# Kernel optimization log

Hardware: AMD Instinct MI355X
Metric: run time of the kernel (lower is better)

The kernel has to match this reference:

```python
import jax, jax.numpy as jnp
import numpy as np

B, L, DIM, H = 2, 2048, 2048, 16
DH = DIM // H  # 128, size_per_head


def setup_inputs() -> dict:
    key = jax.random.key(0)
    k1, k2, k3, k4, k5, k6 = jax.random.split(key, 6)
    s = 0.02
    return {
        "query_tensor": jax.random.normal(k1, (B, L, DIM), jnp.float32),
        "value_tensor": jax.random.normal(k2, (B, L, DIM), jnp.float32),
        "attention_mask": jax.random.randint(k3, (B, L), 0, 2).astype(jnp.float32),
        "Wq": jax.random.normal(k4, (DIM, DIM), jnp.float32) * s,
        "Wk": jax.random.normal(k5, (DIM, DIM), jnp.float32) * s,
        "Wv": jax.random.normal(k6, (DIM, DIM), jnp.float32) * s,
    }


def reference(query_tensor, value_tensor, attention_mask, Wq, Wk, Wv):
    b, lq, dim = query_tensor.shape
    lv = value_tensor.shape[1]
    # torch Linear: x @ W.T (no bias)
    q = query_tensor @ Wq.T   # [B, Lq, DIM]
    k = value_tensor @ Wk.T   # [B, Lv, DIM]
    v = value_tensor @ Wv.T   # [B, Lv, DIM]
    # split heads -> [B, H, L, DH]
    q = q.reshape(b, lq, H, DH).transpose(0, 2, 1, 3)
    k = k.reshape(b, lv, H, DH).transpose(0, 2, 1, 3)
    v = v.reshape(b, lv, H, DH).transpose(0, 2, 1, 3)
    scores = jnp.einsum('bhqd,bhkd->bhqk', q, k) / jnp.sqrt(jnp.float32(DH))
    # multiplicative per-query mask, broadcast [B,1,Lq,1] -> [B,H,Lq,Lv]
    scores = scores * attention_mask[:, None, :, None]
    probs = jax.nn.softmax(scores, axis=-1)
    attn = jnp.einsum('bhqk,bhkd->bhqd', probs, v)  # [B,H,Lq,DH]
    return attn.transpose(0, 2, 1, 3).reshape(b, lq, dim)
```

## Files before the change

### kernel.cpp

```cpp
#include <hip/hip_runtime.h>
#include <hip/hip_bf16.h>
#include <stdint.h>

#define DIM_ 2048
#define L_   2048
#define B_   2
#define H_   16
#define DH_  128
#define NT_  32

#define QSCALE_ 0.12751743f

typedef __attribute__((ext_vector_type(4))) float fp32x4;
typedef __attribute__((ext_vector_type(8))) short s16x8;

__device__ __forceinline__ unsigned short bf16_rne(float f) {
    unsigned u = __builtin_bit_cast(unsigned, f);
    u += 0x7fffu + ((u >> 16) & 1u);
    return (unsigned short)(u >> 16);
}

__device__ __forceinline__ fp32x4 MFMA(s16x8 a, s16x8 b, fp32x4 c) {
    return __builtin_amdgcn_mfma_f32_16x16x32_bf16(a, b, c, 0, 0, 0);
}

__device__ __forceinline__ void gld16(const void* g, void* l) {
    auto gp = reinterpret_cast<const uint32_t __attribute__((address_space(1)))*>(
        reinterpret_cast<uintptr_t>(g));
    auto lp = reinterpret_cast<uint32_t __attribute__((address_space(3)))*>(
        reinterpret_cast<uintptr_t>(l));
    __builtin_amdgcn_global_load_lds(gp, lp, 16, 0, 0);
}

__device__ __forceinline__ float exp2_raw(float x) {
    float r; asm("v_exp_f32 %0, %1" : "=v"(r) : "v"(x)); return r;
}

__device__ __forceinline__ unsigned cvtpk_bf16(float a, float b) {
    unsigned r; asm("v_cvt_pk_bf16_f32 %0, %1, %2" : "=v"(r) : "v"(a), "v"(b)); return r;
}

__global__ void __launch_bounds__(256)
cvt_all(const float* __restrict__ query, const float* __restrict__ value,
        const float* __restrict__ Wq, const float* __restrict__ Wk,
        const float* __restrict__ Wv,
        unsigned short* __restrict__ qb, unsigned short* __restrict__ vb,
        unsigned short* __restrict__ wqb, unsigned short* __restrict__ wkb,
        unsigned short* __restrict__ wvb)
{
    const int total4 = 7340032;
    int i = blockIdx.x * 256 + threadIdx.x;
    const int stride = gridDim.x * 256;
    for (; i < total4; i += stride) {
        const float4* s; ushort4* d; int off; float sc = 1.0f;
        if (i < 2097152)      { s = (const float4*)query; d = (ushort4*)qb;  off = i; }
        else if (i < 4194304) { s = (const float4*)value; d = (ushort4*)vb;  off = i - 2097152; }
        else if (i < 5242880) { s = (const float4*)Wq;    d = (ushort4*)wqb; off = i - 4194304; sc = QSCALE_; }
        else if (i < 6291456) { s = (const float4*)Wk;    d = (ushort4*)wkb; off = i - 5242880; }
        else                  { s = (const float4*)Wv;    d = (ushort4*)wvb; off = i - 6291456; }
        float4 v = s[off];
        ushort4 o;
        o.x = bf16_rne(v.x * sc); o.y = bf16_rne(v.y * sc);
        o.z = bf16_rne(v.z * sc); o.w = bf16_rne(v.w * sc);
        d[off] = o;
    }
}

__global__ void __launch_bounds__(512, 2)
qgemm(const unsigned short* __restrict__ qb, const unsigned short* __restrict__ wqb,
      const float* __restrict__ mask, unsigned short* __restrict__ q_ws)
{
    __shared__ __align__(16) char As_[3][32768];
    __shared__ __align__(16) char Bs_[3][16384];

    const int tid  = threadIdx.x;
    const int lane = tid & 63;
    const int wid  = tid >> 6;
    const int wm   = wid >> 1;
    const int wn   = wid & 1;
    const int lr   = lane & 15;
    const int lg   = lane >> 4;

    const int rb = (blockIdx.x & 7) * 32 + (blockIdx.x >> 3);
    const int bm = (rb >> 4) << 8;
    const int bn = (rb & 15) << 7;

    const int srow = tid >> 3;
    const int scol = ((tid & 7) ^ ((tid >> 3) & 7)) * 8;
    const unsigned short* gA = qb  + (size_t)(bm + srow) * DIM_ + scol;
    const unsigned short* gB = wqb + (size_t)(bn + srow) * DIM_ + scol;
    const int ldst = wid * 1024;

    const int r7   = (lr & 7) << 4;
    const int arow = (wm * 64 + lr) * 128;
    const int brow = (wn * 64 + lr) * 128;
    const int off0 = (lg << 4) ^ r7;
    const int off1 = (64 | (lg << 4)) ^ r7;

    fp32x4 acc[4][4] = {};

#define STG6(SA, SB, T) do {                                                      \
    gld16(gA + (size_t)(T) * 64,                 (SA) + ldst);                    \
    gld16(gA + (size_t)64  * DIM_ + (T) * 64,    (SA) + 8192  + ldst);            \
    gld16(gA + (size_t)128 * DIM_ + (T) * 64,    (SA) + 16384 + ldst);            \
    gld16(gA + (size_t)192 * DIM_ + (T) * 64,    (SA) + 24576 + ldst);            \
    gld16(gB + (size_t)(T) * 64,                 (SB) + ldst);                    \
    gld16(gB + (size_t)64  * DIM_ + (T) * 64,    (SB) + 8192  + ldst);            \
} while (0)

    STG6(&As_[0][0], &Bs_[0][0], 0);
    STG6(&As_[1][0], &Bs_[1][0], 1);
    asm volatile("s_waitcnt vmcnt(6)" ::: "memory");
    __builtin_amdgcn_s_barrier();

    for (int t = 0; t < NT_; ++t) {
        char* Ab = &As_[t % 3][0];
        char* Bb = &Bs_[t % 3][0];
        if (t < NT_ - 2) {
            STG6(&As_[(t + 2) % 3][0], &Bs_[(t + 2) % 3][0], t + 2);
        }

        s16x8 fa0[4], fa1[4], fb0[4], fb1[4];
        #pragma unroll
        for (int mi = 0; mi < 4; ++mi) {
            fa0[mi] = *reinterpret_cast<const s16x8*>(&Ab[arow + mi * 2048 + off0]);
            fa1[mi] = *reinterpret_cast<const s16x8*>(&Ab[arow + mi * 2048 + off1]);
        }
        #pragma unroll
        for (int nf = 0; nf < 4; ++nf) {
            fb0[nf] = *reinterpret_cast<const s16x8*>(&Bb[brow + nf * 2048 + off0]);
            fb1[nf] = *reinterpret_cast<const s16x8*>(&Bb[brow + nf * 2048 + off1]);
        }

        __builtin_amdgcn_s_setprio(1);
        #pragma unroll
        for (int mi = 0; mi < 4; ++mi)
            #pragma unroll
            for (int nf = 0; nf < 4; ++nf)
                acc[mi][nf] = MFMA(fa0[mi], fb0[nf], acc[mi][nf]);
        #pragma unroll
        for (int mi = 0; mi < 4; ++mi)
            #pragma unroll
            for (int nf = 0; nf < 4; ++nf)
                acc[mi][nf] = MFMA(fa1[mi], fb1[nf], acc[mi][nf]);
        __builtin_amdgcn_s_setprio(0);

        if (t < NT_ - 2) {
            asm volatile("s_waitcnt vmcnt(6)" ::: "memory");
            __builtin_amdgcn_s_barrier();
        } else if (t == NT_ - 2) {
            asm volatile("s_waitcnt vmcnt(0)" ::: "memory");
            __builtin_amdgcn_s_barrier();
        }
    }
#undef STG6

    const int bb = bm >> 11;
    const size_t bh0 = (size_t)(bb * H_) * (L_ * DH_);
    const int rbase = bm + wm * 64;
    const int cbase = bn + wn * 64;
    const float* mrow = mask + bb * L_;

    #pragma unroll
    for (int mf = 0; mf < 4; ++mf)
        #pragma unroll
        for (int rr = 0; rr < 4; ++rr) {
            int l = (rbase + mf * 16 + lg * 4 + rr) & (L_ - 1);
            float mvv = mrow[l];
            #pragma unroll
            for (int nf = 0; nf < 4; ++nf) {
                int dc = cbase + nf * 16 + lr;
                int h = dc >> 7, d = dc & 127;
                q_ws[bh0 + (size_t)h * (L_ * DH_) + (size_t)l * DH_ + d]
                    = bf16_rne(acc[mf][nf][rr] * mvv);
            }
        }
}

__global__ void __launch_bounds__(512, 2)
kvgemm(const unsigned short* __restrict__ vb, const unsigned short* __restrict__ wkb,
       const unsigned short* __restrict__ wvb,
       unsigned short* __restrict__ k_ws, unsigned short* __restrict__ v_ws)
{
    __shared__ __align__(16) char As_[2][32768];
    __shared__ __align__(16) char Bks_[2][16384];
    __shared__ __align__(16) char Bvs_[2][16384];

    const int tid  = threadIdx.x;
    const int lane = tid & 63;
    const int wid  = tid >> 6;
    const int wm   = wid >> 1;
    const int wn   = wid & 1;
    const int lr   = lane & 15;
    const int lg   = lane >> 4;

    const int rb = (blockIdx.x & 7) * 32 + (blockIdx.x >> 3);
    const int bm = (rb >> 4) << 8;
    const int bn = (rb & 15) << 7;

    const int srow = tid >> 3;
    const int scol = ((tid & 7) ^ ((tid >> 3) & 7)) * 8;
    const unsigned short* gA  = vb  + (size_t)(bm + srow) * DIM_ + scol;
    const unsigned short* gBk = wkb + (size_t)(bn + srow) * DIM_ + scol;
    const unsigned short* gBv = wvb + (size_t)(bn + srow) * DIM_ + scol;
    const int ldst = wid * 1024;

    const int r7   = (lr & 7) << 4;
    const int arow = (wm * 64 + lr) * 128;
    const int brow = (wn * 64 + lr) * 128;
    const int off0 = (lg << 4) ^ r7;
    const int off1 = (64 | (lg << 4)) ^ r7;

    fp32x4 acck[4][4] = {};
    fp32x4 accv[4][4] = {};

#define STG8(BUF, T) do {                                                         \
    gld16(gA  + (size_t)(T) * 64,               &As_[BUF][ldst]);                 \
    gld16(gA  + (size_t)64  * DIM_ + (T) * 64,  &As_[BUF][8192  + ldst]);         \
    gld16(gA  + (size_t)128 * DIM_ + (T) * 64,  &As_[BUF][16384 + ldst]);         \
    gld16(gA  + (size_t)192 * DIM_ + (T) * 64,  &As_[BUF][24576 + ldst]);         \
    gld16(gBk + (size_t)(T) * 64,               &Bks_[BUF][ldst]);                \
    gld16(gBk + (size_t)64  * DIM_ + (T) * 64,  &Bks_[BUF][8192 + ldst]);         \
    gld16(gBv + (size_t)(T) * 64,               &Bvs_[BUF][ldst]);                \
    gld16(gBv + (size_t)64  * DIM_ + (T) * 64,  &Bvs_[BUF][8192 + ldst]);         \
} while (0)

    STG8(0, 0);
    asm volatile("s_waitcnt vmcnt(0)" ::: "memory");
    __builtin_amdgcn_s_barrier();

    for (int t = 0; t < NT_; ++t) {
        const int buf = t & 1;
        if (t + 1 < NT_) STG8(buf ^ 1, t + 1);

        char* Ab  = &As_[buf][0];
        char* Bkb = &Bks_[buf][0];
        char* Bvb = &Bvs_[buf][0];

        #pragma unroll
        for (int kk = 0; kk < 2; ++kk) {
            const int o = kk ? off1 : off0;
            s16x8 fa[4], fk[4];
            #pragma unroll
            for (int mi = 0; mi < 4; ++mi)
                fa[mi] = *reinterpret_cast<const s16x8*>(&Ab[arow + mi * 2048 + o]);
            #pragma unroll
            for (int nf = 0; nf < 4; ++nf)
                fk[nf] = *reinterpret_cast<const s16x8*>(&Bkb[brow + nf * 2048 + o]);
            __builtin_amdgcn_s_setprio(1);
            #pragma unroll
            for (int mi = 0; mi < 4; ++mi)
                #pragma unroll
                for (int nf = 0; nf < 4; ++nf)
                    acck[mi][nf] = MFMA(fa[mi], fk[nf], acck[mi][nf]);
            __builtin_amdgcn_s_setprio(0);
            s16x8 fv[4];
            #pragma unroll
            for (int nf = 0; nf < 4; ++nf)
                fv[nf] = *reinterpret_cast<const s16x8*>(&Bvb[brow + nf * 2048 + o]);
            __builtin_amdgcn_s_setprio(1);
            #pragma unroll
            for (int mi = 0; mi < 4; ++mi)
                #pragma unroll
                for (int nf = 0; nf < 4; ++nf)
                    accv[mi][nf] = MFMA(fa[mi], fv[nf], accv[mi][nf]);
            __builtin_amdgcn_s_setprio(0);
        }

        if (t + 1 < NT_) {
            asm volatile("s_waitcnt vmcnt(0)" ::: "memory");
            __builtin_amdgcn_s_barrier();
        }
    }
#undef STG8

    const int bb = bm >> 11;
    const size_t bh0 = (size_t)(bb * H_) * (L_ * DH_);
    const int rbase = bm + wm * 64;
    const int cbase = bn + wn * 64;

    #pragma unroll
    for (int mf = 0; mf < 4; ++mf)
        #pragma unroll
        for (int rr = 0; rr < 4; ++rr) {
            int l = (rbase + mf * 16 + lg * 4 + rr) & (L_ - 1);
            #pragma unroll
            for (int nf = 0; nf < 4; ++nf) {
                int dc = cbase + nf * 16 + lr;
                int h = dc >> 7, d = dc & 127;
                size_t off = bh0 + (size_t)h * (L_ * DH_)
                    + (size_t)(((l >> 4) * 4 + (d >> 5)) * 512
                    + ((l & 15) + (((d >> 3) & 3) << 4)) * 8 + (d & 7));
                k_ws[off] = bf16_rne(acck[mf][nf][rr]);
            }
        }

    #pragma unroll
    for (int mf = 0; mf < 4; ++mf) {
        int l0 = (rbase + mf * 16 + lg * 4) & (L_ - 1);
        #pragma unroll
        for (int nf = 0; nf < 4; ++nf) {
            int dc = cbase + nf * 16 + lr;
            int h = dc >> 7, d = dc & 127;
            size_t off = bh0 + (size_t)h * (L_ * DH_)
                + (size_t)(((l0 >> 5) * 8 + (d >> 4)) * 512
                + ((d & 15) + (((l0 >> 3) & 3) << 4)) * 8 + (l0 & 7));
            ushort4 pk;
            pk.x = bf16_rne(accv[mf][nf][0]);
            pk.y = bf16_rne(accv[mf][nf][1]);
            pk.z = bf16_rne(accv[mf][nf][2]);
            pk.w = bf16_rne(accv[mf][nf][3]);
            *reinterpret_cast<ushort4*>(&v_ws[off]) = pk;
        }
    }
}

__global__ void __launch_bounds__(256, 2)
attn_fused3(const unsigned short* __restrict__ qw, const unsigned short* __restrict__ kfr,
            const unsigned short* __restrict__ vfr, float* __restrict__ out)
{
    __shared__ __align__(16) char Ks[2][16384];
    __shared__ __align__(16) char Pl[4][4608];

    const int tid  = threadIdx.x;
    const int lane = tid & 63;
    const int wid  = tid >> 6;
    const int lr   = lane & 15;
    const int lg   = lane >> 4;

    const int p  = (blockIdx.x & 7) * 64 + (blockIdx.x >> 3);
    const int bh = p >> 4;
    const int qt = p & 15;
    const int b  = bh >> 4;
    const int h  = bh & 15;
    const int q0 = qt * 128 + wid * 32;

    const unsigned short* qbase = qw  + (size_t)bh * (L_ * DH_);
    const unsigned short* kbase = kfr + (size_t)bh * (L_ * DH_);
    const unsigned short* vbase = vfr + (size_t)bh * (L_ * DH_);

    s16x8 qf[2][4];
    #pragma unroll
    for (int qs = 0; qs < 2; ++qs)
        #pragma unroll
        for (int kc = 0; kc < 4; ++kc)
            qf[qs][kc] = *reinterpret_cast<const s16x8*>(
                &qbase[(size_t)(q0 + qs * 16 + lr) * DH_ + kc * 32 + lg * 8]);

    s16x8 ones;
    #pragma unroll
    for (int i = 0; i < 8; ++i) ones[i] = (short)0x3F80;

    fp32x4 acc[2][8] = {};
    fp32x4 racc[2] = {};

    char* P = &Pl[wid][0];

    auto STAGE = [&](int buf, int t) {
        const unsigned short* g = kbase + (size_t)t * 8192;
        #pragma unroll
        for (int c = 0; c < 4; ++c)
            gld16(g + c * 2048 + tid * 8, &Ks[buf][c * 4096 + wid * 1024]);
    };

    STAGE(0, 0);
    __syncthreads();

    for (int t = 0; t < L_ / 64; ++t) {
        const int buf = t & 1;
        if (t + 1 < L_ / 64) STAGE(buf ^ 1, t + 1);

        s16x8 vv0[8], vv1[8];
        #pragma unroll
        for (int ds = 0; ds < 8; ++ds)
            vv0[ds] = *reinterpret_cast<const s16x8*>(
                &vbase[(size_t)t * 8192 + (0 * 8 + ds) * 512 + lane * 8]);

        fp32x4 s2[2][4] = {};
        __builtin_amdgcn_s_setprio(1);
        #pragma unroll
        for (int kvs = 0; kvs < 4; ++kvs)
            #pragma unroll
            for (int kc = 0; kc < 4; ++kc) {
                s16x8 kf = *reinterpret_cast<const s16x8*>(
                    Ks[buf] + (kvs * 4 + kc) * 1024 + lane * 16);
                s2[0][kvs] = MFMA(kf, qf[0][kc], s2[0][kvs]);
                s2[1][kvs] = MFMA(kf, qf[1][kc], s2[1][kvs]);
            }
        __builtin_amdgcn_s_setprio(0);

        #pragma unroll
        for (int qs = 0; qs < 2; ++qs)
            #pragma unroll
            for (int kvs = 0; kvs < 4; ++kvs) {
                float e0 = exp2_raw(s2[qs][kvs][0]);
                float e1 = exp2_raw(s2[qs][kvs][1]);
                float e2 = exp2_raw(s2[qs][kvs][2]);
                float e3 = exp2_raw(s2[qs][kvs][3]);
                uint2 pk;
                pk.x = cvtpk_bf16(e0, e1);
                pk.y = cvtpk_bf16(e2, e3);
                *reinterpret_cast<uint2*>(P + qs * 2304 + lr * 144 + kvs * 32 + lg * 8) = pk;
            }

        #pragma unroll
        for (int ds = 0; ds < 8; ++ds)
            vv1[ds] = *reinterpret_cast<const s16x8*>(
                &vbase[(size_t)t * 8192 + (1 * 8 + ds) * 512 + lane * 8]);

        __builtin_amdgcn_s_setprio(1);
        #pragma unroll
        for (int qs = 0; qs < 2; ++qs) {
            s16x8 pa0 = *reinterpret_cast<const s16x8*>(P + qs * 2304 + lr * 144 + 0 * 64 + lg * 16);
            s16x8 pa1 = *reinterpret_cast<const s16x8*>(P + qs * 2304 + lr * 144 + 1 * 64 + lg * 16);
            racc[qs] = MFMA(pa0, ones, racc[qs]);
            racc[qs] = MFMA(pa1, ones, racc[qs]);
            #pragma unroll
            for (int ds = 0; ds < 8; ++ds) {
                acc[qs][ds] = MFMA(pa0, vv0[ds], acc[qs][ds]);
                acc[qs][ds] = MFMA(pa1, vv1[ds], acc[qs][ds]);
            }
        }
        __builtin_amdgcn_s_setprio(0);

        __syncthreads();
    }

    #pragma unroll
    for (int qs = 0; qs < 2; ++qs) {
        float inv[4];
        #pragma unroll
        for (int r = 0; r < 4; ++r) inv[r] = 1.0f / racc[qs][r];
        #pragma unroll
        for (int ds = 0; ds < 8; ++ds)
            #pragma unroll
            for (int r = 0; r < 4; ++r)
                out[((size_t)(b * L_ + q0 + qs * 16 + lg * 4 + r)) * DIM_ + h * DH_ + ds * 16 + lr]
                    = acc[qs][ds][r] * inv[r];
    }
}

extern "C" void kernel_launch(void* const* d_in, const int* in_sizes, int n_in,
                              void* d_out, int out_size, void* d_ws, size_t ws_size,
                              hipStream_t stream) {
    const float* query = (const float*)d_in[0];
    const float* value = (const float*)d_in[1];
    const float* mask  = (const float*)d_in[2];
    const float* Wq    = (const float*)d_in[3];
    const float* Wk    = (const float*)d_in[4];
    const float* Wv    = (const float*)d_in[5];
    float* out = (float*)d_out;

    const size_t elems  = (size_t)B_ * H_ * L_ * DH_;
    const size_t welems = elems / 2;
    unsigned short* q_ws = (unsigned short*)d_ws;
    unsigned short* k_ws = q_ws + elems;
    unsigned short* v_ws = k_ws + elems;

    unsigned short* qbf  = v_ws + elems;
    unsigned short* vbf  = qbf + elems;
    unsigned short* wqbf = vbf + elems;
    unsigned short* wkbf = wqbf + welems;
    unsigned short* wvbf = wkbf + welems;

    dim3 blk(256, 1, 1);

    cvt_all<<<dim3(2048, 1, 1), blk, 0, stream>>>(query, value, Wq, Wk, Wv,
                                                  qbf, vbf, wqbf, wkbf, wvbf);
    qgemm<<<dim3(256, 1, 1), dim3(512, 1, 1), 0, stream>>>(qbf, wqbf, mask, q_ws);
    kvgemm<<<dim3(256, 1, 1), dim3(512, 1, 1), 0, stream>>>(vbf, wkbf, wvbf, k_ws, v_ws);

    attn_fused3<<<dim3(512, 1, 1), blk, 0, stream>>>(q_ws, k_ws, v_ws, out);
}
```

Baseline: 194.1 us.

## Fuse weight fp32-to-bf16 conversion into projection GEMM B-tile loading

Drops the separate conversion of Wq/Wk/Wv to bf16 and has each projection GEMM load fp32 weight tiles into registers, convert them (applying the query scale for Wq), and write swizzled bf16 into LDS. This removes a full read-write pass over the three weight matrices in the conversion kernel. In exchange, the GEMMs read fp32 weights (twice the bytes) and repeat the conversion once per block row. The Q GEMM also drops from a 3-stage async pipeline to 2-stage double buffering with register staging and full __syncthreads, which may expose more load latency.

Result: slower. 203.4 us (+4.8%).

```diff
diff --git a/kernel.cpp b/kernel.cpp
--- a/kernel.cpp
+++ b/kernel.cpp
@@ -41,37 +41,30 @@
 }
 
 __global__ void __launch_bounds__(256)
-cvt_all(const float* __restrict__ query, const float* __restrict__ value,
-        const float* __restrict__ Wq, const float* __restrict__ Wk,
-        const float* __restrict__ Wv,
-        unsigned short* __restrict__ qb, unsigned short* __restrict__ vb,
-        unsigned short* __restrict__ wqb, unsigned short* __restrict__ wkb,
-        unsigned short* __restrict__ wvb)
+cvt_qv(const float* __restrict__ query, const float* __restrict__ value,
+       unsigned short* __restrict__ qb, unsigned short* __restrict__ vb)
 {
-    const int total4 = 7340032;
+    const int total4 = 4194304;
     int i = blockIdx.x * 256 + threadIdx.x;
     const int stride = gridDim.x * 256;
     for (; i < total4; i += stride) {
-        const float4* s; ushort4* d; int off; float sc = 1.0f;
-        if (i < 2097152)      { s = (const float4*)query; d = (ushort4*)qb;  off = i; }
-        else if (i < 4194304) { s = (const float4*)value; d = (ushort4*)vb;  off = i - 2097152; }
-        else if (i < 5242880) { s = (const float4*)Wq;    d = (ushort4*)wqb; off = i - 4194304; sc = QSCALE_; }
-        else if (i < 6291456) { s = (const float4*)Wk;    d = (ushort4*)wkb; off = i - 5242880; }
-        else                  { s = (const float4*)Wv;    d = (ushort4*)wvb; off = i - 6291456; }
+        const float4* s; ushort4* d; int off;
+        if (i < 2097152) { s = (const float4*)query; d = (ushort4*)qb; off = i; }
+        else             { s = (const float4*)value; d = (ushort4*)vb; off = i - 2097152; }
         float4 v = s[off];
         ushort4 o;
-        o.x = bf16_rne(v.x * sc); o.y = bf16_rne(v.y * sc);
-        o.z = bf16_rne(v.z * sc); o.w = bf16_rne(v.w * sc);
+        o.x = bf16_rne(v.x); o.y = bf16_rne(v.y);
+        o.z = bf16_rne(v.z); o.w = bf16_rne(v.w);
         d[off] = o;
     }
 }
 
 __global__ void __launch_bounds__(512, 2)
-qgemm(const unsigned short* __restrict__ qb, const unsigned short* __restrict__ wqb,
+qgemm(const unsigned short* __restrict__ qb, const float* __restrict__ Wq,
       const float* __restrict__ mask, unsigned short* __restrict__ q_ws)
 {
-    __shared__ __align__(16) char As_[3][32768];
-    __shared__ __align__(16) char Bs_[3][16384];
+    __shared__ __align__(16) char As_[2][32768];
+    __shared__ __align__(16) char Bs_[2][16384];
 
     const int tid  = threadIdx.x;
     const int lane = tid & 63;
@@ -87,9 +80,15 @@
 
     const int srow = tid >> 3;
     const int scol = ((tid & 7) ^ ((tid >> 3) & 7)) * 8;
-    const unsigned short* gA = qb  + (size_t)(bm + srow) * DIM_ + scol;
-    const unsigned short* gB = wqb + (size_t)(bn + srow) * DIM_ + scol;
+    const unsigned short* gA = qb + (size_t)(bm + srow) * DIM_ + scol;
     const int ldst = wid * 1024;
+
+    const int brow_s = tid >> 2;
+    const int bks    = (tid & 3) * 16;
+    const float* gBW = Wq + (size_t)(bn + brow_s) * DIM_ + bks;
+    const int bch0 = (tid & 3) * 2;
+    const int baddr0 = brow_s * 128 + ((bch0 ^ (brow_s & 7)) << 4);
+    const int baddr1 = brow_s * 128 + (((bch0 + 1) ^ (brow_s & 7)) << 4);
 
     const int r7   = (lr & 7) << 4;
     const int arow = (wm * 64 + lr) * 128;
@@ -99,37 +98,59 @@
 
     fp32x4 acc[4][4] = {};
 
-#define STG6(SA, SB, T) do {                                                      \
-    gld16(gA + (size_t)(T) * 64,                 (SA) + ldst);                    \
-    gld16(gA + (size_t)64  * DIM_ + (T) * 64,    (SA) + 8192  + ldst);            \
-    gld16(gA + (size_t)128 * DIM_ + (T) * 64,    (SA) + 16384 + ldst);            \
-    gld16(gA + (size_t)192 * DIM_ + (T) * 64,    (SA) + 24576 + ldst);            \
-    gld16(gB + (size_t)(T) * 64,                 (SB) + ldst);                    \
-    gld16(gB + (size_t)64  * DIM_ + (T) * 64,    (SB) + 8192  + ldst);            \
+#define STGA(BUF, T) do {                                                         \
+    gld16(gA + (size_t)(T) * 64,                 &As_[BUF][ldst]);                \
+    gld16(gA + (size_t)64  * DIM_ + (T) * 64,    &As_[BUF][8192  + ldst]);        \
+    gld16(gA + (size_t)128 * DIM_ + (T) * 64,    &As_[BUF][16384 + ldst]);        \
+    gld16(gA + (size_t)192 * DIM_ + (T) * 64,    &As_[BUF][24576 + ldst]);        \
 } while (0)
 
-    STG6(&As_[0][0], &Bs_[0][0], 0);
-    STG6(&As_[1][0], &Bs_[1][0], 1);
-    asm volatile("s_waitcnt vmcnt(6)" ::: "memory");
-    __builtin_amdgcn_s_barrier();
+#define LOADB(T) do {                                                             \
+    b4[0] = *reinterpret_cast<const float4*>(gBW + (size_t)(T) * 64);             \
+    b4[1] = *reinterpret_cast<const float4*>(gBW + (size_t)(T) * 64 + 4);         \
+    b4[2] = *reinterpret_cast<const float4*>(gBW + (size_t)(T) * 64 + 8);         \
+    b4[3] = *reinterpret_cast<const float4*>(gBW + (size_t)(T) * 64 + 12);        \
+} while (0)
+
+#define WRITEB(BUF) do {                                                          \
+    uint2 p0, p1;                                                                 \
+    p0.x = cvtpk_bf16(b4[0].x * QSCALE_, b4[0].y * QSCALE_);                      \
+    p0.y = cvtpk_bf16(b4[0].z * QSCALE_, b4[0].w * QSCALE_);                      \
+    p1.x = cvtpk_bf16(b4[1].x * QSCALE_, b4[1].y * QSCALE_);                      \
+    p1.y = cvtpk_bf16(b4[1].z * QSCALE_, b4[1].w * QSCALE_);                      \
+    *reinterpret_cast<uint2*>(&Bs_[BUF][baddr0])     = p0;                        \
+    *reinterpret_cast<uint2*>(&Bs_[BUF][baddr0 + 8]) = p1;                        \
+    p0.x = cvtpk_bf16(b4[2].x * QSCALE_, b4[2].y * QSCALE_);                      \
+    p0.y = cvtpk_bf16(b4[2].z * QSCALE_, b4[2].w * QSCALE_);                      \
+    p1.x = cvtpk_bf16(b4[3].x * QSCALE_, b4[3].y * QSCALE_);                      \
+    p1.y = cvtpk_bf16(b4[3].z * QSCALE_, b4[3].w * QSCALE_);                      \
+    *reinterpret_cast<uint2*>(&Bs_[BUF][baddr1])     = p0;                        \
+    *reinterpret_cast<uint2*>(&Bs_[BUF][baddr1 + 8]) = p1;                        \
+} while (0)
+
+    float4 b4[4];
+    STGA(0, 0);
+    LOADB(0);
+    WRITEB(0);
+    __syncthreads();
 
     for (int t = 0; t < NT_; ++t) {
-        char* Ab = &As_[t % 3][0];
-        char* Bb = &Bs_[t % 3][0];
-        if (t < NT_ - 2) {
-            STG6(&As_[(t + 2) % 3][0], &Bs_[(t + 2) % 3][0], t + 2);
+        const int buf = t & 1;
+        if (t + 1 < NT_) {
+            STGA(buf ^ 1, t + 1);
+            LOADB(t + 1);
         }
 
         s16x8 fa0[4], fa1[4], fb0[4], fb1[4];
         #pragma unroll
         for (int mi = 0; mi < 4; ++mi) {
-            fa0[mi] = *reinterpret_cast<const s16x8*>(&Ab[arow + mi * 2048 + off0]);
-            fa1[mi] = *reinterpret_cast<const s16x8*>(&Ab[arow + mi * 2048 + off1]);
+            fa0[mi] = *reinterpret_cast<const s16x8*>(&As_[buf][arow + mi * 2048 + off0]);
+            fa1[mi] = *reinterpret_cast<const s16x8*>(&As_[buf][arow + mi * 2048 + off1]);
         }
         #pragma unroll
         for (int nf = 0; nf < 4; ++nf) {
-            fb0[nf] = *reinterpret_cast<const s16x8*>(&Bb[brow + nf * 2048 + off0]);
-            fb1[nf] = *reinterpret_cast<const s16x8*>(&Bb[brow + nf * 2048 + off1]);
+            fb0[nf] = *reinterpret_cast<const s16x8*>(&Bs_[buf][brow + nf * 2048 + off0]);
+            fb1[nf] = *reinterpret_cast<const s16x8*>(&Bs_[buf][brow + nf * 2048 + off1]);
         }
 
         __builtin_amdgcn_s_setprio(1);
@@ -145,15 +166,12 @@
                 acc[mi][nf] = MFMA(fa1[mi], fb1[nf], acc[mi][nf]);
         __builtin_amdgcn_s_setprio(0);
 
-        if (t < NT_ - 2) {
-            asm volatile("s_waitcnt vmcnt(6)" ::: "memory");
-            __builtin_amdgcn_s_barrier();
-        } else if (t == NT_ - 2) {
-            asm volatile("s_waitcnt vmcnt(0)" ::: "memory");
-            __builtin_amdgcn_s_barrier();
-        }
+        if (t + 1 < NT_) WRITEB(buf ^ 1);
+        __syncthreads();
     }
-#undef STG6
+#undef STGA
+#undef LOADB
+#undef WRITEB
 
     const int bb = bm >> 11;
     const size_t bh0 = (size_t)(bb * H_) * (L_ * DH_);
@@ -178,8 +196,8 @@
 }
 
 __global__ void __launch_bounds__(512, 2)
-kvgemm(const unsigned short* __restrict__ vb, const unsigned short* __restrict__ wkb,
-       const unsigned short* __restrict__ wvb,
+kvgemm(const unsigned short* __restrict__ vb, const float* __restrict__ Wk,
+       const float* __restrict__ Wv,
        unsigned short* __restrict__ k_ws, unsigned short* __restrict__ v_ws)
 {
     __shared__ __align__(16) char As_[2][32768];
@@ -200,10 +218,16 @@
 
     const int srow = tid >> 3;
     const int scol = ((tid & 7) ^ ((tid >> 3) & 7)) * 8;
-    const unsigned short* gA  = vb  + (size_t)(bm + srow) * DIM_ + scol;
-    const unsigned short* gBk = wkb + (size_t)(bn + srow) * DIM_ + scol;
-    const unsigned short* gBv = wvb + (size_t)(bn + srow) * DIM_ + scol;
+    const unsigned short* gA = vb + (size_t)(bm + srow) * DIM_ + scol;
     const int ldst = wid * 1024;
+
+    const int brow_s = tid >> 2;
+    const int bks    = (tid & 3) * 16;
+    const float* gBk = Wk + (size_t)(bn + brow_s) * DIM_ + bks;
+    const float* gBv = Wv + (size_t)(bn + brow_s) * DIM_ + bks;
+    const int bch0 = (tid & 3) * 2;
+    const int baddr0 = brow_s * 128 + ((bch0 ^ (brow_s & 7)) << 4);
+    const int baddr1 = brow_s * 128 + (((bch0 + 1) ^ (brow_s & 7)) << 4);
 
     const int r7   = (lr & 7) << 4;
     const int arow = (wm * 64 + lr) * 128;
@@ -214,28 +238,56 @@
     fp32x4 acck[4][4] = {};
     fp32x4 accv[4][4] = {};
 
-#define STG8(BUF, T) do {                                                         \
-    gld16(gA  + (size_t)(T) * 64,               &As_[BUF][ldst]);                 \
-    gld16(gA  + (size_t)64  * DIM_ + (T) * 64,  &As_[BUF][8192  + ldst]);         \
-    gld16(gA  + (size_t)128 * DIM_ + (T) * 64,  &As_[BUF][16384 + ldst]);         \
-    gld16(gA  + (size_t)192 * DIM_ + (T) * 64,  &As_[BUF][24576 + ldst]);         \
-    gld16(gBk + (size_t)(T) * 64,               &Bks_[BUF][ldst]);                \
-    gld16(gBk + (size_t)64  * DIM_ + (T) * 64,  &Bks_[BUF][8192 + ldst]);         \
-    gld16(gBv + (size_t)(T) * 64,               &Bvs_[BUF][ldst]);                \
-    gld16(gBv + (size_t)64  * DIM_ + (T) * 64,  &Bvs_[BUF][8192 + ldst]);         \
+#define STGA(BUF, T) do {                                                         \
+    gld16(gA + (size_t)(T) * 64,                 &As_[BUF][ldst]);                \
+    gld16(gA + (size_t)64  * DIM_ + (T) * 64,    &As_[BUF][8192  + ldst]);        \
+    gld16(gA + (size_t)128 * DIM_ + (T) * 64,    &As_[BUF][16384 + ldst]);        \
+    gld16(gA + (size_t)192 * DIM_ + (T) * 64,    &As_[BUF][24576 + ldst]);        \
 } while (0)
 
-    STG8(0, 0);
-    asm volatile("s_waitcnt vmcnt(0)" ::: "memory");
-    __builtin_amdgcn_s_barrier();
+#define LOADB2(T) do {                                                            \
+    k4[0] = *reinterpret_cast<const float4*>(gBk + (size_t)(T) * 64);             \
+    k4[1] = *reinterpret_cast<const float4*>(gBk + (size_t)(T) * 64 + 4);         \
+    k4[2] = *reinterpret_cast<const float4*>(gBk + (size_t)(T) * 64 + 8);         \
+    k4[3] = *reinterpret_cast<const float4*>(gBk + (size_t)(T) * 64 + 12);        \
+    v4[0] = *reinterpret_cast<const float4*>(gBv + (size_t)(T) * 64);             \
+    v4[1] = *reinterpret_cast<const float4*>(gBv + (size_t)(T) * 64 + 4);         \
+    v4[2] = *reinterpret_cast<const float4*>(gBv + (size_t)(T) * 64 + 8);         \
+    v4[3] = *reinterpret_cast<const float4*>(gBv + (size_t)(T) * 64 + 12);        \
+} while (0)
+
+#define WRITEB2(BUF) do {                                                         \
+    uint2 p0, p1;                                                                 \
+    p0.x = cvtpk_bf16(k4[0].x, k4[0].y); p0.y = cvtpk_bf16(k4[0].z, k4[0].w);     \
+    p1.x = cvtpk_bf16(k4[1].x, k4[1].y); p1.y = cvtpk_bf16(k4[1].z, k4[1].w);     \
+    *reinterpret_cast<uint2*>(&Bks_[BUF][baddr0])     = p0;                       \
+    *reinterpret_cast<uint2*>(&Bks_[BUF][baddr0 + 8]) = p1;                       \
+    p0.x = cvtpk_bf16(k4[2].x, k4[2].y); p0.y = cvtpk_bf16(k4[2].z, k4[2].w);     \
+    p1.x = cvtpk_bf16(k4[3].x, k4[3].y); p1.y = cvtpk_bf16(k4[3].z, k4[3].w);     \
+    *reinterpret_cast<uint2*>(&Bks_[BUF][baddr1])     = p0;                       \
+    *reinterpret_cast<uint2*>(&Bks_[BUF][baddr1 + 8]) = p1;                       \
+    p0.x = cvtpk_bf16(v4[0].x, v4[0].y); p0.y = cvtpk_bf16(v4[0].z, v4[0].w);     \
+    p1.x = cvtpk_bf16(v4[1].x, v4[1].y); p1.y = cvtpk_bf16(v4[1].z, v4[1].w);     \
+    *reinterpret_cast<uint2*>(&Bvs_[BUF][baddr0])     = p0;                       \
+    *reinterpret_cast<uint2*>(&Bvs_[BUF][baddr0 + 8]) = p1;                       \
+    p0.x = cvtpk_bf16(v4[2].x, v4[2].y); p0.y = cvtpk_bf16(v4[2].z, v4[2].w);     \
+    p1.x = cvtpk_bf16(v4[3].x, v4[3].y); p1.y = cvtpk_bf16(v4[3].z, v4[3].w);     \
+    *reinterpret_cast<uint2*>(&Bvs_[BUF][baddr1])     = p0;                       \
+    *reinterpret_cast<uint2*>(&Bvs_[BUF][baddr1 + 8]) = p1;                       \
+} while (0)
+
+    float4 k4[4], v4[4];
+    STGA(0, 0);
+    LOADB2(0);
+    WRITEB2(0);
+    __syncthreads();
 
     for (int t = 0; t < NT_; ++t) {
         const int buf = t & 1;
-        if (t + 1 < NT_) STG8(buf ^ 1, t + 1);
-
-        char* Ab  = &As_[buf][0];
-        char* Bkb = &Bks_[buf][0];
-        char* Bvb = &Bvs_[buf][0];
+        if (t + 1 < NT_) {
+            STGA(buf ^ 1, t + 1);
+            LOADB2(t + 1);
+        }
 
         #pragma unroll
         for (int kk = 0; kk < 2; ++kk) {
@@ -243,10 +295,10 @@
             s16x8 fa[4], fk[4];
             #pragma unroll
             for (int mi = 0; mi < 4; ++mi)
-                fa[mi] = *reinterpret_cast<const s16x8*>(&Ab[arow + mi * 2048 + o]);
+                fa[mi] = *reinterpret_cast<const s16x8*>(&As_[buf][arow + mi * 2048 + o]);
             #pragma unroll
             for (int nf = 0; nf < 4; ++nf)
-                fk[nf] = *reinterpret_cast<const s16x8*>(&Bkb[brow + nf * 2048 + o]);
+                fk[nf] = *reinterpret_cast<const s16x8*>(&Bks_[buf][brow + nf * 2048 + o]);
             __builtin_amdgcn_s_setprio(1);
             #pragma unroll
             for (int mi = 0; mi < 4; ++mi)
@@ -257,7 +309,7 @@
             s16x8 fv[4];
             #pragma unroll
             for (int nf = 0; nf < 4; ++nf)
-                fv[nf] = *reinterpret_cast<const s16x8*>(&Bvb[brow + nf * 2048 + o]);
+                fv[nf] = *reinterpret_cast<const s16x8*>(&Bvs_[buf][brow + nf * 2048 + o]);
             __builtin_amdgcn_s_setprio(1);
             #pragma unroll
             for (int mi = 0; mi < 4; ++mi)
@@ -267,12 +319,12 @@
             __builtin_amdgcn_s_setprio(0);
         }
 
-        if (t + 1 < NT_) {
-            asm volatile("s_waitcnt vmcnt(0)" ::: "memory");
-            __builtin_amdgcn_s_barrier();
-        }
+        if (t + 1 < NT_) WRITEB2(buf ^ 1);
+        __syncthreads();
     }
-#undef STG8
+#undef STGA
+#undef LOADB2
+#undef WRITEB2
 
     const int bb = bm >> 11;
     const size_t bh0 = (size_t)(bb * H_) * (L_ * DH_);
@@ -451,24 +503,18 @@
     const float* Wv    = (const float*)d_in[5];
     float* out = (float*)d_out;
 
-    const size_t elems  = (size_t)B_ * H_ * L_ * DH_;
-    const size_t welems = elems / 2;
+    const size_t elems = (size_t)B_ * H_ * L_ * DH_;
     unsigned short* q_ws = (unsigned short*)d_ws;
     unsigned short* k_ws = q_ws + elems;
     unsigned short* v_ws = k_ws + elems;
-
     unsigned short* qbf  = v_ws + elems;
     unsigned short* vbf  = qbf + elems;
-    unsigned short* wqbf = vbf + elems;
-    unsigned short* wkbf = wqbf + welems;
-    unsigned short* wvbf = wkbf + welems;
 
     dim3 blk(256, 1, 1);
 
-    cvt_all<<<dim3(2048, 1, 1), blk, 0, stream>>>(query, value, Wq, Wk, Wv,
-                                                  qbf, vbf, wqbf, wkbf, wvbf);
-    qgemm<<<dim3(256, 1, 1), dim3(512, 1, 1), 0, stream>>>(qbf, wqbf, mask, q_ws);
-    kvgemm<<<dim3(256, 1, 1), dim3(512, 1, 1), 0, stream>>>(vbf, wkbf, wvbf, k_ws, v_ws);
+    cvt_qv<<<dim3(2048, 1, 1), blk, 0, stream>>>(query, value, qbf, vbf);
+    qgemm<<<dim3(256, 1, 1), dim3(512, 1, 1), 0, stream>>>(qbf, Wq, mask, q_ws);
+    kvgemm<<<dim3(256, 1, 1), dim3(512, 1, 1), 0, stream>>>(vbf, Wk, Wv, k_ws, v_ws);
 
     attn_fused3<<<dim3(512, 1, 1), blk, 0, stream>>>(q_ws, k_ws, v_ws, out);
 }
```

## Switch attention to 32x32x16 MFMA with register-resident P via permlane swaps

Applied to the files above, without the earlier changes.

Rewrites the attention kernel to use 32x32x16 bf16 MFMA tiles instead of 16x16x32, and changes the K/V workspace fragment layouts written by the projection GEMM to match. The exponentiated scores are packed into PV A-operands directly in registers using v_permlane32_swap, which removes the per-wave LDS round trip for P. The aim is to cut LDS traffic and instruction count and to get better MFMA efficiency. In exchange it depends on correct lane permutations and new layouts, and it changes register pressure.

Measured after the change: 206.2 us. +6.3%, slower.

```diff
diff --git a/kernel.cpp b/kernel.cpp
--- a/kernel.cpp
+++ b/kernel.cpp
@@ -11,8 +11,10 @@
 
 #define QSCALE_ 0.12751743f
 
-typedef __attribute__((ext_vector_type(4))) float fp32x4;
-typedef __attribute__((ext_vector_type(8))) short s16x8;
+typedef __attribute__((ext_vector_type(4)))  float    fp32x4;
+typedef __attribute__((ext_vector_type(16))) float    fp32x16;
+typedef __attribute__((ext_vector_type(8)))  short    s16x8;
+typedef __attribute__((ext_vector_type(4)))  unsigned u32x4;
 
 __device__ __forceinline__ unsigned short bf16_rne(float f) {
     unsigned u = __builtin_bit_cast(unsigned, f);
@@ -22,6 +24,10 @@
 
 __device__ __forceinline__ fp32x4 MFMA(s16x8 a, s16x8 b, fp32x4 c) {
     return __builtin_amdgcn_mfma_f32_16x16x32_bf16(a, b, c, 0, 0, 0);
+}
+
+__device__ __forceinline__ fp32x16 MFMA32(s16x8 a, s16x8 b, fp32x16 c) {
+    return __builtin_amdgcn_mfma_f32_32x32x16_bf16(a, b, c, 0, 0, 0);
 }
 
 __device__ __forceinline__ void gld16(const void* g, void* l) {
@@ -38,6 +44,10 @@
 
 __device__ __forceinline__ unsigned cvtpk_bf16(float a, float b) {
     unsigned r; asm("v_cvt_pk_bf16_f32 %0, %1, %2" : "=v"(r) : "v"(a), "v"(b)); return r;
+}
+
+__device__ __forceinline__ void swap32(unsigned &a, unsigned &b) {
+    asm volatile("v_permlane32_swap_b32 %0, %1" : "+v"(a), "+v"(b));
 }
 
 __global__ void __launch_bounds__(256)
@@ -284,13 +294,15 @@
         #pragma unroll
         for (int rr = 0; rr < 4; ++rr) {
             int l = (rbase + mf * 16 + lg * 4 + rr) & (L_ - 1);
+            int r = l & 63;
             #pragma unroll
             for (int nf = 0; nf < 4; ++nf) {
                 int dc = cbase + nf * 16 + lr;
                 int h = dc >> 7, d = dc & 127;
                 size_t off = bh0 + (size_t)h * (L_ * DH_)
-                    + (size_t)(((l >> 4) * 4 + (d >> 5)) * 512
-                    + ((l & 15) + (((d >> 3) & 3) << 4)) * 8 + (d & 7));
+                    + (size_t)((l >> 6) * 8192
+                    + ((r >> 5) * 8 + (d >> 4)) * 512
+                    + ((d >> 3) & 1) * 256 + (r & 31) * 8 + (d & 7));
                 k_ws[off] = bf16_rne(acck[mf][nf][rr]);
             }
         }
@@ -298,13 +310,15 @@
     #pragma unroll
     for (int mf = 0; mf < 4; ++mf) {
         int l0 = (rbase + mf * 16 + lg * 4) & (L_ - 1);
+        int r0 = l0 & 63;
         #pragma unroll
         for (int nf = 0; nf < 4; ++nf) {
             int dc = cbase + nf * 16 + lr;
             int h = dc >> 7, d = dc & 127;
             size_t off = bh0 + (size_t)h * (L_ * DH_)
-                + (size_t)(((l0 >> 5) * 8 + (d >> 4)) * 512
-                + ((d & 15) + (((l0 >> 3) & 3) << 4)) * 8 + (l0 & 7));
+                + (size_t)((l0 >> 6) * 8192
+                + ((r0 >> 4) * 4 + (d >> 5)) * 512
+                + ((r0 >> 3) & 1) * 256 + (d & 31) * 8 + (r0 & 7));
             ushort4 pk;
             pk.x = bf16_rne(accv[mf][nf][0]);
             pk.y = bf16_rne(accv[mf][nf][1]);
@@ -316,17 +330,16 @@
 }
 
 __global__ void __launch_bounds__(256, 2)
-attn_fused3(const unsigned short* __restrict__ qw, const unsigned short* __restrict__ kfr,
+attn_fused7(const unsigned short* __restrict__ qw, const unsigned short* __restrict__ kfr,
             const unsigned short* __restrict__ vfr, float* __restrict__ out)
 {
     __shared__ __align__(16) char Ks[2][16384];
-    __shared__ __align__(16) char Pl[4][4608];
 
     const int tid  = threadIdx.x;
     const int lane = tid & 63;
     const int wid  = tid >> 6;
-    const int lr   = lane & 15;
-    const int lg   = lane >> 4;
+    const int l31  = lane & 31;
+    const int hi   = lane >> 5;
 
     const int p  = (blockIdx.x & 7) * 64 + (blockIdx.x >> 3);
     const int bh = p >> 4;
@@ -339,22 +352,18 @@
     const unsigned short* kbase = kfr + (size_t)bh * (L_ * DH_);
     const unsigned short* vbase = vfr + (size_t)bh * (L_ * DH_);
 
-    s16x8 qf[2][4];
-    #pragma unroll
-    for (int qs = 0; qs < 2; ++qs)
-        #pragma unroll
-        for (int kc = 0; kc < 4; ++kc)
-            qf[qs][kc] = *reinterpret_cast<const s16x8*>(
-                &qbase[(size_t)(q0 + qs * 16 + lr) * DH_ + kc * 32 + lg * 8]);
+    s16x8 qf[8];
+    #pragma unroll
+    for (int ks = 0; ks < 8; ++ks)
+        qf[ks] = *reinterpret_cast<const s16x8*>(
+            &qbase[(size_t)(q0 + l31) * DH_ + ks * 16 + hi * 8]);
 
     s16x8 ones;
     #pragma unroll
     for (int i = 0; i < 8; ++i) ones[i] = (short)0x3F80;
 
-    fp32x4 acc[2][8] = {};
-    fp32x4 racc[2] = {};
-
-    char* P = &Pl[wid][0];
+    fp32x16 acc[4] = {};
+    fp32x16 racc = {};
 
     auto STAGE = [&](int buf, int t) {
         const unsigned short* g = kbase + (size_t)t * 8192;
@@ -363,81 +372,87 @@
             gld16(g + c * 2048 + tid * 8, &Ks[buf][c * 4096 + wid * 1024]);
     };
 
+    auto pack2 = [&](const fp32x16& s, s16x8& paA, s16x8& paB) {
+        unsigned c01   = cvtpk_bf16(exp2_raw(s[0]),  exp2_raw(s[1]));
+        unsigned c23   = cvtpk_bf16(exp2_raw(s[2]),  exp2_raw(s[3]));
+        unsigned c89   = cvtpk_bf16(exp2_raw(s[4]),  exp2_raw(s[5]));
+        unsigned c1011 = cvtpk_bf16(exp2_raw(s[6]),  exp2_raw(s[7]));
+        swap32(c01, c89);
+        swap32(c23, c1011);
+        paA = __builtin_bit_cast(s16x8, (u32x4){c01, c23, c89, c1011});
+        unsigned d01   = cvtpk_bf16(exp2_raw(s[8]),  exp2_raw(s[9]));
+        unsigned d23   = cvtpk_bf16(exp2_raw(s[10]), exp2_raw(s[11]));
+        unsigned d89   = cvtpk_bf16(exp2_raw(s[12]), exp2_raw(s[13]));
+        unsigned d1011 = cvtpk_bf16(exp2_raw(s[14]), exp2_raw(s[15]));
+        swap32(d01, d89);
+        swap32(d23, d1011);
+        paB = __builtin_bit_cast(s16x8, (u32x4){d01, d23, d89, d1011});
+    };
+
     STAGE(0, 0);
     __syncthreads();
 
-    for (int t = 0; t < L_ / 64; ++t) {
+    for (int t = 0; t < NT_; ++t) {
         const int buf = t & 1;
-        if (t + 1 < L_ / 64) STAGE(buf ^ 1, t + 1);
-
-        s16x8 vv0[8], vv1[8];
-        #pragma unroll
-        for (int ds = 0; ds < 8; ++ds)
-            vv0[ds] = *reinterpret_cast<const s16x8*>(
-                &vbase[(size_t)t * 8192 + (0 * 8 + ds) * 512 + lane * 8]);
-
-        fp32x4 s2[2][4] = {};
+        if (t + 1 < NT_) STAGE(buf ^ 1, t + 1);
+        const size_t tb = (size_t)t * 8192;
+
+        s16x8 vf[8];
+        #pragma unroll
+        for (int f = 0; f < 8; ++f)
+            vf[f] = *reinterpret_cast<const s16x8*>(&vbase[tb + f * 512 + lane * 8]);
+
+        fp32x16 s0 = {}, s1 = {};
         __builtin_amdgcn_s_setprio(1);
         #pragma unroll
-        for (int kvs = 0; kvs < 4; ++kvs)
-            #pragma unroll
-            for (int kc = 0; kc < 4; ++kc) {
-                s16x8 kf = *reinterpret_cast<const s16x8*>(
-                    Ks[buf] + (kvs * 4 + kc) * 1024 + lane * 16);
-                s2[0][kvs] = MFMA(kf, qf[0][kc], s2[0][kvs]);
-                s2[1][kvs] = MFMA(kf, qf[1][kc], s2[1][kvs]);
-            }
+        for (int ks = 0; ks < 8; ++ks) {
+            s16x8 k0 = *reinterpret_cast<const s16x8*>(Ks[buf] + ks * 1024 + lane * 16);
+            s16x8 k1 = *reinterpret_cast<const s16x8*>(Ks[buf] + (8 + ks) * 1024 + lane * 16);
+            s0 = MFMA32(k0, qf[ks], s0);
+            s1 = MFMA32(k1, qf[ks], s1);
+        }
         __builtin_amdgcn_s_setprio(0);
 
-        #pragma unroll
-        for (int qs = 0; qs < 2; ++qs)
-            #pragma unroll
-            for (int kvs = 0; kvs < 4; ++kvs) {
-                float e0 = exp2_raw(s2[qs][kvs][0]);
-                float e1 = exp2_raw(s2[qs][kvs][1]);
-                float e2 = exp2_raw(s2[qs][kvs][2]);
-                float e3 = exp2_raw(s2[qs][kvs][3]);
-                uint2 pk;
-                pk.x = cvtpk_bf16(e0, e1);
-                pk.y = cvtpk_bf16(e2, e3);
-                *reinterpret_cast<uint2*>(P + qs * 2304 + lr * 144 + kvs * 32 + lg * 8) = pk;
-            }
-
-        #pragma unroll
-        for (int ds = 0; ds < 8; ++ds)
-            vv1[ds] = *reinterpret_cast<const s16x8*>(
-                &vbase[(size_t)t * 8192 + (1 * 8 + ds) * 512 + lane * 8]);
+        s16x8 pa0, pa1, pa2, pa3;
+        pack2(s0, pa0, pa1);
+        pack2(s1, pa2, pa3);
 
         __builtin_amdgcn_s_setprio(1);
-        #pragma unroll
-        for (int qs = 0; qs < 2; ++qs) {
-            s16x8 pa0 = *reinterpret_cast<const s16x8*>(P + qs * 2304 + lr * 144 + 0 * 64 + lg * 16);
-            s16x8 pa1 = *reinterpret_cast<const s16x8*>(P + qs * 2304 + lr * 144 + 1 * 64 + lg * 16);
-            racc[qs] = MFMA(pa0, ones, racc[qs]);
-            racc[qs] = MFMA(pa1, ones, racc[qs]);
-            #pragma unroll
-            for (int ds = 0; ds < 8; ++ds) {
-                acc[qs][ds] = MFMA(pa0, vv0[ds], acc[qs][ds]);
-                acc[qs][ds] = MFMA(pa1, vv1[ds], acc[qs][ds]);
-            }
-        }
+        racc = MFMA32(pa0, ones, racc);
+        racc = MFMA32(pa1, ones, racc);
+        #pragma unroll
+        for (int db = 0; db < 4; ++db) acc[db] = MFMA32(pa0, vf[db], acc[db]);
+        #pragma unroll
+        for (int db = 0; db < 4; ++db) acc[db] = MFMA32(pa1, vf[4 + db], acc[db]);
+        __builtin_amdgcn_s_setprio(0);
+
+        #pragma unroll
+        for (int f = 0; f < 8; ++f)
+            vf[f] = *reinterpret_cast<const s16x8*>(&vbase[tb + (8 + f) * 512 + lane * 8]);
+
+        __builtin_amdgcn_s_setprio(1);
+        racc = MFMA32(pa2, ones, racc);
+        racc = MFMA32(pa3, ones, racc);
+        #pragma unroll
+        for (int db = 0; db < 4; ++db) acc[db] = MFMA32(pa2, vf[db], acc[db]);
+        #pragma unroll
+        for (int db = 0; db < 4; ++db) acc[db] = MFMA32(pa3, vf[4 + db], acc[db]);
         __builtin_amdgcn_s_setprio(0);
 
         __syncthreads();
     }
 
-    #pragma unroll
-    for (int qs = 0; qs < 2; ++qs) {
-        float inv[4];
-        #pragma unroll
-        for (int r = 0; r < 4; ++r) inv[r] = 1.0f / racc[qs][r];
-        #pragma unroll
-        for (int ds = 0; ds < 8; ++ds)
-            #pragma unroll
-            for (int r = 0; r < 4; ++r)
-                out[((size_t)(b * L_ + q0 + qs * 16 + lg * 4 + r)) * DIM_ + h * DH_ + ds * 16 + lr]
-                    = acc[qs][ds][r] * inv[r];
-    }
+    float inv[16];
+    #pragma unroll
+    for (int r = 0; r < 16; ++r) inv[r] = 1.0f / racc[r];
+    #pragma unroll
+    for (int db = 0; db < 4; ++db)
+        #pragma unroll
+        for (int r = 0; r < 16; ++r) {
+            int q = q0 + (r & 3) + 8 * (r >> 2) + 4 * hi;
+            out[((size_t)(b * L_ + q)) * DIM_ + h * DH_ + db * 32 + l31]
+                = acc[db][r] * inv[r];
+        }
 }
 
 extern "C" void kernel_launch(void* const* d_in, const int* in_sizes, int n_in,
@@ -470,5 +485,5 @@
     qgemm<<<dim3(256, 1, 1), dim3(512, 1, 1), 0, stream>>>(qbf, wqbf, mask, q_ws);
     kvgemm<<<dim3(256, 1, 1), dim3(512, 1, 1), 0, stream>>>(vbf, wkbf, wvbf, k_ws, v_ws);
 
-    attn_fused3<<<dim3(512, 1, 1), blk, 0, stream>>>(q_ws, k_ws, v_ws, out);
-}
+    attn_fused7<<<dim3(512, 1, 1), blk, 0, stream>>>(q_ws, k_ws, v_ws, out);
+}
```
